# Performance work log

Measured on AMD Instinct MI355X. Metric: run time of the kernel, lower is better.

Reference implementation:

```python
import jax, jax.numpy as jnp
import numpy as np

HIDDEN_DIM = 2048
NUM_EXPERTS = 64
TOP_K = 8
NUM_TOKENS = 16384


def setup_inputs() -> dict:
    key = jax.random.key(0)
    k_x, k_w, k_b = jax.random.split(key, 3)
    X = jax.random.normal(k_x, (NUM_TOKENS, HIDDEN_DIM), dtype=jnp.float32)
    # nn.Linear(hidden_dim, num_experts): weight [out, in], bias [out]
    bound = 1.0 / np.sqrt(HIDDEN_DIM)
    W_gate = jax.random.uniform(k_w, (NUM_EXPERTS, HIDDEN_DIM), jnp.float32, -bound, bound)
    b_gate = jax.random.uniform(k_b, (NUM_EXPERTS,), jnp.float32, -bound, bound)
    return {"X": X, "W_gate": W_gate, "b_gate": b_gate}


def reference(X, W_gate, b_gate):
    # gate linear: [T, H] @ [H, E] + [E] -> [T, E]
    router_logits = jnp.einsum('th,eh->te', X, W_gate) + b_gate
    # softmax in float32 (matches dtype=torch.float)
    router_probs = jax.nn.softmax(router_logits.astype(jnp.float32), axis=-1)
    # top-k over experts: [T, K]
    router_weights, selected_experts_indices = jax.lax.top_k(router_probs, TOP_K)
    router_weights = router_weights / jnp.sum(router_weights, axis=-1, keepdims=True)
    router_weights = router_weights.astype(X.dtype)
    # one-hot [T, K, E] -> permute(2,1,0) -> [E, K, T]
    expert_mask = jax.nn.one_hot(selected_experts_indices, NUM_EXPERTS, dtype=jnp.int64 if jax.config.jax_enable_x64 else jnp.int32)
    expert_mask = jnp.transpose(expert_mask, (2, 1, 0))
    return (router_logits, router_weights, selected_experts_indices.astype(jnp.int32), expert_mask)
```

## Files before the change

kernel.cpp:

```cpp
#include <hip/hip_runtime.h>

#define NT 16384
#define NH 2048
#define NE 64
#define TOPK 8

#define TB 32
#define NSS 16

#define LOFF 0
#define WOFF (NT * NE)
#define IOFF (WOFF + NT * TOPK)
#define MOFF (IOFF + NT * TOPK)

typedef __attribute__((ext_vector_type(8))) short short8;
typedef __attribute__((ext_vector_type(16))) float floatx16;

union FragU { uint4 u; short8 s; };

__device__ __forceinline__ void glds16(const void* g, void* l) {
    __builtin_amdgcn_global_load_lds(
        (const __attribute__((address_space(1))) unsigned int*)g,
        (__attribute__((address_space(3))) unsigned int*)l, 16, 0, 0);
}

__device__ __forceinline__ unsigned pack3(float a, float b, unsigned& w1, unsigned& w2) {
    unsigned au = __float_as_uint(a), bu = __float_as_uint(b);
    unsigned ah0 = au & 0xFFFF0000u, bh0 = bu & 0xFFFF0000u;
    float ra = a - __uint_as_float(ah0);
    float rb = b - __uint_as_float(bh0);
    unsigned ar = __float_as_uint(ra), br = __float_as_uint(rb);
    unsigned ah1 = ar & 0xFFFF0000u, bh1 = br & 0xFFFF0000u;
    float sa = ra - __uint_as_float(ah1);
    float sb = rb - __uint_as_float(bh1);
    w1 = bh1 | (ah1 >> 16);
    w2 = (__float_as_uint(sb) & 0xFFFF0000u) | (__float_as_uint(sa) >> 16);
    return bh0 | (ah0 >> 16);
}

__global__ __launch_bounds__(256)
void prep_kernel(const float* __restrict__ Wg, uint4* __restrict__ wsp,
                 float* __restrict__ out) {
    const int b = blockIdx.x;
    const int tid = threadIdx.x;

    float4 z = make_float4(0.f, 0.f, 0.f, 0.f);
    float4* mp = (float4*)(out + MOFF) + (size_t)b * 8192 + tid;
#pragma unroll
    for (int it = 0; it < 32; it++) mp[it * 256] = z;

    if (tid < 64) {
        const int t = b >> 2, g = (b >> 1) & 1, h = b & 1;
        const int l = tid;
        const int e  = g * 32 + (l & 31);
        const int k0 = t * 32 + h * 16 + (l >> 5) * 8;
        const float* src = Wg + (size_t)e * NH + k0;
        float4 w0 = *(const float4*)src;
        float4 w1 = *(const float4*)(src + 4);
        unsigned u1[4], u2[4];
        uint4 p0;
        p0.x = pack3(w0.x, w0.y, u1[0], u2[0]);
        p0.y = pack3(w0.z, w0.w, u1[1], u2[1]);
        p0.z = pack3(w1.x, w1.y, u1[2], u2[2]);
        p0.w = pack3(w1.z, w1.w, u1[3], u2[3]);
        const size_t idx0 = (size_t)((t * 2 + g) * 3) * 2 + h;
        uint4* dst = wsp + idx0 * 64 + l;
        dst[0]   = p0;
        dst[128] = make_uint4(u1[0], u1[1], u1[2], u1[3]);
        dst[256] = make_uint4(u2[0], u2[1], u2[2], u2[3]);
    }
}

__global__ __launch_bounds__(512, 4)
void gemm_kernel(const float* __restrict__ X, const uint4* __restrict__ wsp,
                 const float* __restrict__ bg, float* __restrict__ out) {
    __shared__ float XS[2][4][32][32];
    __shared__ float P[4][TB][68];

    const int tid = threadIdx.x;
    const int wv  = tid >> 6;
    const int l   = tid & 63;
    const int eh  = wv & 1;
    const int kq  = wv >> 1;
    const int l31 = l & 31;
    const int lh  = l >> 5;
    const int tbase = blockIdx.x * TB;

    floatx16 acc = (floatx16)0.0f;

    const int j0 = wv * 2, j1 = wv * 2 + 1;
    const int q0 = j0 >> 2, r80 = (j0 & 3) * 8;
    const int q1 = j1 >> 2, r81 = (j1 & 3) * 8;
    const float* src0 = X + (size_t)(tbase + r80 + (l >> 3)) * NH + q0 * 512
                          + (((l & 7) ^ ((l >> 3) & 7)) << 2);
    const float* src1 = X + (size_t)(tbase + r81 + (l >> 3)) * NH + q1 * 512
                          + (((l & 7) ^ ((l >> 3) & 7)) << 2);

#define STAGE(ss_, s_) do { \
    glds16(src0 + (ss_) * 32, &XS[s_][q0][r80][0]); \
    glds16(src1 + (ss_) * 32, &XS[s_][q1][r81][0]); \
} while (0)

    STAGE(0, 0);
    __syncthreads();

#pragma unroll 2
    for (int t = 0; t < NSS; t++) {
        const int slot = t & 1;
        const int T = kq * NSS + t;
        const uint4* bt = wsp + (size_t)((T * 2 + eh) * 6) * 64 + l;

        if (t + 1 < NSS) STAGE(t + 1, slot ^ 1);

        const float* xr = &XS[slot][kq][l31][0];
        const int s7 = l & 7;
        const int gb = lh * 2;

#pragma unroll
        for (int h = 0; h < 2; h++) {
            FragU b0, b1, b2;
            b0.u = bt[(0 * 2 + h) * 64];
            b1.u = bt[(1 * 2 + h) * 64];
            b2.u = bt[(2 * 2 + h) * 64];

            float4 r0 = *(const float4*)(xr + (((gb + 4 * h) ^ s7) << 2));
            float4 r1 = *(const float4*)(xr + (((gb + 4 * h + 1) ^ s7) << 2));

            FragU a0, a1, a2;
            {
                unsigned u1[4], u2[4];
                uint4 q;
                q.x = pack3(r0.x, r0.y, u1[0], u2[0]);
                q.y = pack3(r0.z, r0.w, u1[1], u2[1]);
                q.z = pack3(r1.x, r1.y, u1[2], u2[2]);
                q.w = pack3(r1.z, r1.w, u1[3], u2[3]);
                a0.u = q;
                a1.u = make_uint4(u1[0], u1[1], u1[2], u1[3]);
                a2.u = make_uint4(u2[0], u2[1], u2[2], u2[3]);
            }

            __builtin_amdgcn_s_setprio(1);
            acc = __builtin_amdgcn_mfma_f32_32x32x16_bf16(a0.s, b0.s, acc, 0, 0, 0);
            acc = __builtin_amdgcn_mfma_f32_32x32x16_bf16(a0.s, b1.s, acc, 0, 0, 0);
            acc = __builtin_amdgcn_mfma_f32_32x32x16_bf16(a1.s, b0.s, acc, 0, 0, 0);
            acc = __builtin_amdgcn_mfma_f32_32x32x16_bf16(a1.s, b1.s, acc, 0, 0, 0);
            acc = __builtin_amdgcn_mfma_f32_32x32x16_bf16(a0.s, b2.s, acc, 0, 0, 0);
            acc = __builtin_amdgcn_mfma_f32_32x32x16_bf16(a2.s, b0.s, acc, 0, 0, 0);
            __builtin_amdgcn_s_setprio(0);
        }
        __syncthreads();
    }

#pragma unroll
    for (int r = 0; r < 16; r++)
        P[kq][(r & 3) + 8 * (r >> 2) + 4 * lh][eh * 32 + l31] = acc[r];
    __syncthreads();

    {
        const int tok = tid >> 4;
        const int e4  = (tid & 15) << 2;
        float4 s0 = *(const float4*)&P[0][tok][e4];
        float4 s1 = *(const float4*)&P[1][tok][e4];
        float4 s2 = *(const float4*)&P[2][tok][e4];
        float4 s3 = *(const float4*)&P[3][tok][e4];
        float4 bb = *(const float4*)(bg + e4);
        float4 v;
        v.x = s0.x + s1.x + s2.x + s3.x + bb.x;
        v.y = s0.y + s1.y + s2.y + s3.y + bb.y;
        v.z = s0.z + s1.z + s2.z + s3.z + bb.z;
        v.w = s0.w + s1.w + s2.w + s3.w + bb.w;
        *(float4*)(out + LOFF + (size_t)(tbase + tok) * NE + e4) = v;
    }
}

__global__ __launch_bounds__(512)
void topk_kernel(const float* __restrict__ out_logits, float* __restrict__ out) {
    const int tid = threadIdx.x;
    const int tok = blockIdx.x * 64 + (tid >> 3);
    const int el  = tid & 7;
    const float* lrow = out_logits + (size_t)tok * NE + el * 8;
    float4 va = *(const float4*)lrow;
    float4 vb = *(const float4*)(lrow + 4);
    float v[8] = {va.x, va.y, va.z, va.w, vb.x, vb.y, vb.z, vb.w};

    unsigned msk = 0;
    float m0 = 0.f, ssum = 0.f, myv = 0.f;
    int myi = 0;
#pragma unroll
    for (int r = 0; r < 8; r++) {
        float bv = -3.0e38f; int bi = 64;
#pragma unroll
        for (int j = 0; j < 8; j++) {
            bool better = (((msk >> j) & 1u) == 0u) && (v[j] > bv);
            bv = better ? v[j] : bv;
            bi = better ? (el * 8 + j) : bi;
        }
#pragma unroll
        for (int s2 = 1; s2 < 8; s2 <<= 1) {
            float ov = __shfl_xor(bv, s2);
            int   oi = __shfl_xor(bi, s2);
            bool take = (ov > bv) || (ov == bv && oi < bi);
            bv = take ? ov : bv;
            bi = take ? oi : bi;
        }
        if ((bi >> 3) == el) msk |= (1u << (bi & 7));
        if (r == 0) m0 = bv;
        ssum += __expf(bv - m0);
        if (r == el) { myv = bv; myi = bi; }
    }
    float wgt = __expf(myv - m0) / ssum;
    size_t gt = (size_t)tok;
    out[WOFF + gt * TOPK + el] = wgt;
    out[IOFF + gt * TOPK + el] = (float)myi;
    out[MOFF + (size_t)myi * (TOPK * NT) + (size_t)el * NT + gt] = 1.0f;
}

extern "C" void kernel_launch(void* const* d_in, const int* in_sizes, int n_in,
                              void* d_out, int out_size, void* d_ws, size_t ws_size,
                              hipStream_t stream) {
    const float* X  = (const float*)d_in[0];
    const float* Wg = (const float*)d_in[1];
    const float* bg = (const float*)d_in[2];
    float* out = (float*)d_out;
    uint4* wsp = (uint4*)d_ws;

    hipLaunchKernelGGL(prep_kernel, dim3(256), dim3(256), 0, stream, Wg, wsp, out);
    hipLaunchKernelGGL(gemm_kernel, dim3(NT / TB), dim3(512), 0, stream,
                       X, (const uint4*)wsp, bg, out);
    hipLaunchKernelGGL(topk_kernel, dim3(NT / 64), dim3(512), 0, stream,
                       out + LOFF, out);
}
```

Measured before the change: 224.0 us.

## Prefetch packed weight fragments one stage ahead with manual vmcnt waits

```diff
diff --git a/kernel.cpp b/kernel.cpp
--- a/kernel.cpp
+++ b/kernel.cpp
@@ -17,6 +17,8 @@
 typedef __attribute__((ext_vector_type(16))) float floatx16;
 
 union FragU { uint4 u; short8 s; };
+
+#define WAITVM(n) asm volatile("s_waitcnt vmcnt(" #n ")" ::: "memory")
 
 __device__ __forceinline__ void glds16(const void* g, void* l) {
     __builtin_amdgcn_global_load_lds(
@@ -101,55 +103,62 @@
     glds16(src1 + (ss_) * 32, &XS[s_][q1][r81][0]); \
 } while (0)
 
+#define BPREF(dst_, t_) do { \
+    const uint4* bt_ = wsp + (size_t)(((kq * NSS + (t_)) * 2 + eh) * 6) * 64 + l; \
+    dst_[0].u = bt_[0];   dst_[1].u = bt_[64];  dst_[2].u = bt_[128]; \
+    dst_[3].u = bt_[192]; dst_[4].u = bt_[256]; dst_[5].u = bt_[320]; \
+} while (0)
+
+#define CONSUME(slot_, bb_) do { \
+    const float* xr_ = &XS[slot_][kq][l31][0]; \
+    const int s7_ = l & 7; \
+    const int gb_ = lh * 2; \
+    _Pragma("unroll") \
+    for (int h_ = 0; h_ < 2; h_++) { \
+        float4 r0_ = *(const float4*)(xr_ + (((gb_ + 4 * h_) ^ s7_) << 2)); \
+        float4 r1_ = *(const float4*)(xr_ + (((gb_ + 4 * h_ + 1) ^ s7_) << 2)); \
+        FragU a0_, a1_, a2_; \
+        { unsigned u1_[4], u2_[4]; uint4 q_; \
+          q_.x = pack3(r0_.x, r0_.y, u1_[0], u2_[0]); \
+          q_.y = pack3(r0_.z, r0_.w, u1_[1], u2_[1]); \
+          q_.z = pack3(r1_.x, r1_.y, u1_[2], u2_[2]); \
+          q_.w = pack3(r1_.z, r1_.w, u1_[3], u2_[3]); \
+          a0_.u = q_; \
+          a1_.u = make_uint4(u1_[0], u1_[1], u1_[2], u1_[3]); \
+          a2_.u = make_uint4(u2_[0], u2_[1], u2_[2], u2_[3]); } \
+        __builtin_amdgcn_s_setprio(1); \
+        acc = __builtin_amdgcn_mfma_f32_32x32x16_bf16(a0_.s, bb_[0 + h_].s, acc, 0, 0, 0); \
+        acc = __builtin_amdgcn_mfma_f32_32x32x16_bf16(a0_.s, bb_[2 + h_].s, acc, 0, 0, 0); \
+        acc = __builtin_amdgcn_mfma_f32_32x32x16_bf16(a1_.s, bb_[0 + h_].s, acc, 0, 0, 0); \
+        acc = __builtin_amdgcn_mfma_f32_32x32x16_bf16(a1_.s, bb_[2 + h_].s, acc, 0, 0, 0); \
+        acc = __builtin_amdgcn_mfma_f32_32x32x16_bf16(a0_.s, bb_[4 + h_].s, acc, 0, 0, 0); \
+        acc = __builtin_amdgcn_mfma_f32_32x32x16_bf16(a2_.s, bb_[0 + h_].s, acc, 0, 0, 0); \
+        __builtin_amdgcn_s_setprio(0); \
+    } \
+} while (0)
+
+    FragU bc[6], bn[6];
+
+    BPREF(bc, 0);
     STAGE(0, 0);
+
+#pragma unroll 2
+    for (int t = 0; t < NSS - 1; t++) {
+        const int slot = t & 1;
+        BPREF(bn, t + 1);
+        STAGE(t + 1, slot ^ 1);
+        WAITVM(8);
+        __builtin_amdgcn_s_barrier();
+        CONSUME(slot, bc);
+        __builtin_amdgcn_s_barrier();
+#pragma unroll
+        for (int i = 0; i < 6; i++) bc[i] = bn[i];
+    }
+    WAITVM(0);
+    __builtin_amdgcn_s_barrier();
+    CONSUME((NSS - 1) & 1, bc);
+
     __syncthreads();
-
-#pragma unroll 2
-    for (int t = 0; t < NSS; t++) {
-        const int slot = t & 1;
-        const int T = kq * NSS + t;
-        const uint4* bt = wsp + (size_t)((T * 2 + eh) * 6) * 64 + l;
-
-        if (t + 1 < NSS) STAGE(t + 1, slot ^ 1);
-
-        const float* xr = &XS[slot][kq][l31][0];
-        const int s7 = l & 7;
-        const int gb = lh * 2;
-
-#pragma unroll
-        for (int h = 0; h < 2; h++) {
-            FragU b0, b1, b2;
-            b0.u = bt[(0 * 2 + h) * 64];
-            b1.u = bt[(1 * 2 + h) * 64];
-            b2.u = bt[(2 * 2 + h) * 64];
-
-            float4 r0 = *(const float4*)(xr + (((gb + 4 * h) ^ s7) << 2));
-            float4 r1 = *(const float4*)(xr + (((gb + 4 * h + 1) ^ s7) << 2));
-
-            FragU a0, a1, a2;
-            {
-                unsigned u1[4], u2[4];
-                uint4 q;
-                q.x = pack3(r0.x, r0.y, u1[0], u2[0]);
-                q.y = pack3(r0.z, r0.w, u1[1], u2[1]);
-                q.z = pack3(r1.x, r1.y, u1[2], u2[2]);
-                q.w = pack3(r1.z, r1.w, u1[3], u2[3]);
-                a0.u = q;
-                a1.u = make_uint4(u1[0], u1[1], u1[2], u1[3]);
-                a2.u = make_uint4(u2[0], u2[1], u2[2], u2[3]);
-            }
-
-            __builtin_amdgcn_s_setprio(1);
-            acc = __builtin_amdgcn_mfma_f32_32x32x16_bf16(a0.s, b0.s, acc, 0, 0, 0);
-            acc = __builtin_amdgcn_mfma_f32_32x32x16_bf16(a0.s, b1.s, acc, 0, 0, 0);
-            acc = __builtin_amdgcn_mfma_f32_32x32x16_bf16(a1.s, b0.s, acc, 0, 0, 0);
-            acc = __builtin_amdgcn_mfma_f32_32x32x16_bf16(a1.s, b1.s, acc, 0, 0, 0);
-            acc = __builtin_amdgcn_mfma_f32_32x32x16_bf16(a0.s, b2.s, acc, 0, 0, 0);
-            acc = __builtin_amdgcn_mfma_f32_32x32x16_bf16(a2.s, b0.s, acc, 0, 0, 0);
-            __builtin_amdgcn_s_setprio(0);
-        }
-        __syncthreads();
-    }
 
 #pragma unroll
     for (int r = 0; r < 16; r++)
```

Result: no change. 223.4 us (-0.3%).
